# Optimization experiments

Measured on AMD Instinct MI355X. Metric: run time of the kernel, lower is better.

The kernel has to match this reference:

```python
import jax, jax.numpy as jnp
import numpy as np

B, T, I, H, L = 128, 512, 64, 512, 64  # batch, seq_len, input=latent size, hidden
DEC_STEPS = 100  # hardcoded in the original decoder loop


def _lstm_cell(x, h, c, Wih, Whh, bih, bhh):
    # PyTorch gate order: i, f, g, o
    gates = x @ Wih.T + h @ Whh.T + bih + bhh  # [B, 4H]
    i, f, g, o = jnp.split(gates, 4, axis=-1)
    c = jax.nn.sigmoid(f) * c + jax.nn.sigmoid(i) * jnp.tanh(g)
    h = jax.nn.sigmoid(o) * jnp.tanh(c)
    return h, c


def setup_inputs() -> dict:
    key = jax.random.key(0)
    ks = jax.random.split(key, 18)
    u = lambda k, shape, fan: jax.random.uniform(k, shape, jnp.float32, -1.0, 1.0) / np.sqrt(fan).astype(np.float32)
    return {
        "sequences": jax.random.normal(ks[0], (B, T, I), jnp.float32),
        "seq_lengths": jnp.full((B,), T, dtype=jnp.int32),
        "eps": jax.random.normal(ks[1], (B, L), jnp.float32),
        "W_ih_enc": u(ks[2], (4 * H, I), H), "W_hh_enc": u(ks[3], (4 * H, H), H),
        "b_ih_enc": u(ks[4], (4 * H,), H), "b_hh_enc": u(ks[5], (4 * H,), H),
        "W_mean": u(ks[6], (L, H), H), "b_mean": u(ks[7], (L,), H),
        "W_logvar": u(ks[8], (L, H), H), "b_logvar": u(ks[9], (L,), H),
        "W_init": u(ks[10], (H, L), L), "b_init": u(ks[11], (H,), L),
        "W_ih_dec": u(ks[12], (4 * H, I), H), "W_hh_dec": u(ks[13], (4 * H, H), H),
        "b_ih_dec": u(ks[14], (4 * H,), H), "b_hh_dec": u(ks[15], (4 * H,), H),
        "W_out": u(ks[16], (I, H), H), "b_out": u(ks[17], (I,), H),
    }


def _forward(sequences, eps,
             W_ih_enc, W_hh_enc, b_ih_enc, b_hh_enc,
             W_mean, b_mean, W_logvar, b_logvar,
             W_init, b_init,
             W_ih_dec, W_hh_dec, b_ih_dec, b_hh_dec,
             W_out, b_out):
    Bn = sequences.shape[0]
    h0 = jnp.zeros((Bn, H), sequences.dtype)

    # ---- encoder: full-sequence LSTM, keep only final hidden state ----
    def enc_step(carry, x_t):
        h, c = carry
        h, c = _lstm_cell(x_t, h, c, W_ih_enc, W_hh_enc, b_ih_enc, b_hh_enc)
        return (h, c), None

    (h_n, _), _ = jax.lax.scan(enc_step, (h0, h0), sequences.transpose(1, 0, 2))

    # ---- VAE reparameterization ----
    mean = h_n @ W_mean.T + b_mean
    log_var = h_n @ W_logvar.T + b_logvar
    z = mean + eps * jnp.exp(0.5 * log_var)

    h_dec = z @ W_init.T + b_init
    c_dec = jnp.zeros_like(h_dec)
    x0 = jnp.zeros((Bn, L), z.dtype)

    def dec_step(carry, _):
        h, c, x = carry
        h, c = _lstm_cell(x, h, c, W_ih_dec, W_hh_dec, b_ih_dec, b_hh_dec)
        x_hat = h @ W_out.T + b_out
        return (h, c, x_hat), x_hat

    _, xs = jax.lax.scan(dec_step, (h_dec, c_dec, x0), None, length=DEC_STEPS)
    x_hat = xs.transpose(1, 0, 2)  # [B, 100, I]
    return x_hat, mean, log_var


def reference(sequences, seq_lengths, eps,
              W_ih_enc, W_hh_enc, b_ih_enc, b_hh_enc,
              W_mean, b_mean, W_logvar, b_logvar,
              W_init, b_init,
              W_ih_dec, W_hh_dec, b_ih_dec, b_hh_dec,
              W_out, b_out):
    del seq_lengths  # accepted but unused by the original forward
    return _forward(sequences, eps,
                    W_ih_enc, W_hh_enc, b_ih_enc, b_hh_enc,
                    W_mean, b_mean, W_logvar, b_logvar,
                    W_init, b_init,
                    W_ih_dec, W_hh_dec, b_ih_dec, b_hh_dec,
                    W_out, b_out)
```

## Files before the change

kernel.cpp:

```cpp
#include <hip/hip_runtime.h>
#include <stdint.h>


typedef short short8 __attribute__((ext_vector_type(8)));
typedef float f32x4 __attribute__((ext_vector_type(4)));
typedef unsigned int u32x4 __attribute__((ext_vector_type(4)));

#define WS_FLAGS  0
#define WS_HBUF0  16384
#define WS_HBUF1  147456
#define WS_Z      278528
#define WS_BCOMB  311296
#define WS_WCOMB  319488
#define WS_SEQB   2416640
#define WS_END    10805248
#define WS_ZERO   WS_HBUF1
#define HB1_SIZE  131072

static __device__ __forceinline__ float b2f(unsigned short u) {
    return __builtin_bit_cast(float, (unsigned int)u << 16);
}
static __device__ __forceinline__ unsigned short f2b(float f) {
    unsigned int u = __builtin_bit_cast(unsigned int, f);
    unsigned int r = u + 0x7FFFu + ((u >> 16) & 1u);
    return (unsigned short)(r >> 16);
}
static __device__ __forceinline__ float sigm(float x)  { return 1.0f / (1.0f + __expf(-x)); }
static __device__ __forceinline__ float tanhx(float x) { return 1.0f - 2.0f / (__expf(2.0f * x) + 1.0f); }

static __device__ __forceinline__ short8 cvt8(const float* p) {
    const float4 a = ((const float4*)p)[0];
    const float4 b = ((const float4*)p)[1];
    short8 r;
    r[0] = (short)f2b(a.x); r[1] = (short)f2b(a.y);
    r[2] = (short)f2b(a.z); r[3] = (short)f2b(a.w);
    r[4] = (short)f2b(b.x); r[5] = (short)f2b(b.y);
    r[6] = (short)f2b(b.z); r[7] = (short)f2b(b.w);
    return r;
}

static __device__ __forceinline__ uint32_t phase_of(uint32_t R) {
    return (R <= 512u) ? ((R >> 1) & 1u)
                       : ((((R - 513u) >> 1) & 1u) ^ 1u);
}

static __device__ __forceinline__ int alperm(int u) { return u ^ ((u >> 3) & 7); }

static __device__ __forceinline__ void load2x16_cc(const void* p0, const void* p1,
                                                   u32x4& v0, u32x4& v1) {
    asm volatile("global_load_dwordx4 %0, %2, off sc0 sc1\n\t"
                 "global_load_dwordx4 %1, %3, off sc0 sc1\n\t"
                 "s_waitcnt vmcnt(0)"
                 : "=&v"(v0), "=&v"(v1) : "v"(p0), "v"(p1) : "memory");
}
static __device__ __forceinline__ void store16_cc(void* p, u32x4 v) {
    asm volatile("global_store_dwordx4 %0, %1, off sc0 sc1"
                 :: "v"(p), "v"(v) : "memory");
}
static __device__ __forceinline__ void drain_vm() {
    asm volatile("s_waitcnt vmcnt(0)" ::: "memory");
}

__global__ void __launch_bounds__(256)
seqcvt_kernel(const float* __restrict__ src, unsigned short* __restrict__ dst)
{
    int i = (blockIdx.x * 256 + threadIdx.x) * 4;
    float4 v = *(const float4*)(src + i);
    uint32_t lo = (uint32_t)f2b(v.x) | ((uint32_t)f2b(v.y) << 16);
    uint32_t hi = (uint32_t)f2b(v.z) | ((uint32_t)f2b(v.w) << 16);
    uint2 o; o.x = lo; o.y = hi;
    *(uint2*)(dst + i) = o;
}

__global__ void __launch_bounds__(256)
wcomb_kernel(const float* __restrict__ Wih_d,
             const float* __restrict__ Whh_d,
             const float* __restrict__ Wout,
             const float* __restrict__ bih_d,
             const float* __restrict__ bhh_d,
             const float* __restrict__ bout,
             unsigned char* __restrict__ ws)
{
    __shared__ float Ash[64][64];
    __shared__ float Bsh[64][65];
    const int bid = blockIdx.x, t = threadIdx.x;
    const int gt0 = (bid >> 3) * 64, ht0 = (bid & 7) * 64;
    for (int j = 0; j < 16; ++j) {
        int idx = t + j * 256;
        int r = idx >> 6, c = idx & 63;
        Ash[r][c] = Wih_d[(size_t)(gt0 + r) * 64 + c];
        Bsh[r][c] = Wout[(size_t)r * 512 + ht0 + c];
    }
    __syncthreads();
    const int gl = t >> 2, hl0 = (t & 3) * 16;
    for (int hh = 0; hh < 16; ++hh) {
        float acc = 0.f;
        #pragma unroll
        for (int i = 0; i < 64; ++i) acc += Ash[gl][i] * Bsh[i][hl0 + hh];
        int g = gt0 + gl, h = ht0 + hl0 + hh;
        float v = Whh_d[(size_t)g * 512 + h] + acc;
        ((unsigned short*)(ws + WS_WCOMB))[(size_t)g * 512 + h] = f2b(v);
    }
    if ((bid & 7) == 0 && t < 64) {
        int g = gt0 + t;
        float acc = bih_d[g] + bhh_d[g];
        #pragma unroll
        for (int i = 0; i < 64; ++i) acc += bout[i] * Ash[t][i];
        ((float*)(ws + WS_BCOMB))[g] = acc;
    }
}

__global__ void __launch_bounds__(512, 2)
vae_persistent(const float* __restrict__ seq,
               const unsigned short* __restrict__ seqb,
               const float* __restrict__ eps,
               const float* __restrict__ Wih_e,
               const float* __restrict__ Whh_e,
               const float* __restrict__ bih_e,
               const float* __restrict__ bhh_e,
               const float* __restrict__ Wmean,
               const float* __restrict__ bmean,
               const float* __restrict__ Wlv,
               const float* __restrict__ blv,
               const float* __restrict__ Winit,
               const float* __restrict__ binit,
               const float* __restrict__ Whh_d,
               const float* __restrict__ bih_d,
               const float* __restrict__ bhh_d,
               const float* __restrict__ Wout,
               const float* __restrict__ bout,
               unsigned char* __restrict__ ws,
               float* __restrict__ out)
{
    __shared__ __align__(16) short Al[16 * 520];
    __shared__ __align__(16) short Ho[16 * 36];
    __shared__ float fbuf[128];
    __shared__ float zl[16 * 64];

    const int tid  = threadIdx.x;
    const int g    = blockIdx.x & 7;
    const int s    = blockIdx.x >> 3;
    const int b0   = g * 16;
    const int lane = tid & 63;
    const int wv   = tid >> 6;
    const int col  = lane & 15;
    const int q    = lane >> 4;
    const int nloc = wv * 16 + col;
    const int gt   = nloc & 3;
    const int grow = gt * 512 + s * 32 + (nloc >> 2);

    uint32_t* flags = (uint32_t*)(ws + WS_FLAGS) + (size_t)g * 512;
    unsigned char* hbuf0 = ws + WS_HBUF0;
    unsigned char* hbuf1 = ws + WS_HBUF1;
    uint32_t* zbuf = (uint32_t*)(ws + WS_Z);

    float cst[4] = {0.f, 0.f, 0.f, 0.f};

    int aoff[16];
    #pragma unroll
    for (int kt = 0; kt < 16; ++kt)
        aoff[kt] = col * 520 + alperm(kt * 4 + q) * 8;
    const int stg_b  = tid >> 5;
    const int stg_c  = tid & 31;
    const int stg_u0 = alperm(stg_c * 2);

    auto wait_and_stage = [&](uint32_t R, bool guard) {
        if (guard) __syncthreads();
        const unsigned char* src = (R & 1) ? hbuf1 : hbuf0;
        const uint32_t pm = phase_of(R) ? 0x40004000u : 0u;
        const unsigned char* p0 = src + (size_t)(b0 + stg_b) * 1024 + stg_c * 32;
        u32x4 v0, v1;
        uint32_t tries = 0;
        for (;;) {
            load2x16_cc(p0, p0 + 16, v0, v1);
            uint32_t bad = 0;
            #pragma unroll
            for (int i = 0; i < 4; ++i) {
                bad |= (v0[i] & 0x40004000u) ^ pm;
                bad |= (v1[i] & 0x40004000u) ^ pm;
            }
            if (bad == 0) break;
            if (tries == 1)      __builtin_amdgcn_s_sleep(1);
            else if (tries == 2) __builtin_amdgcn_s_sleep(2);
            else if (tries == 3 || tries == 4) __builtin_amdgcn_s_sleep(4);
            else if (tries >= 5) __builtin_amdgcn_s_sleep(8);
            ++tries;
        }
        #pragma unroll
        for (int i = 0; i < 4; ++i) { v0[i] ^= pm; v1[i] ^= pm; }
        u32x4* dst = (u32x4*)Al;
        dst[stg_b * 65 + stg_u0]       = v0;
        dst[stg_b * 65 + (stg_u0 ^ 1)] = v1;
        __syncthreads();
    };

    auto publish_h = [&](uint32_t R) {
        if (wv == 0) {
            unsigned char* dst = (R & 1) ? hbuf1 : hbuf0;
            const uint32_t pm = phase_of(R) ? 0x40004000u : 0u;
            int row = lane >> 2, part = lane & 3;
            const short* hp = Ho + row * 36 + part * 8;
            uint2 lo = *(const uint2*)(hp);
            uint2 hi = *(const uint2*)(hp + 4);
            u32x4 v; v[0] = lo.x; v[1] = lo.y; v[2] = hi.x; v[3] = hi.y;
            #pragma unroll
            for (int i = 0; i < 4; ++i) v[i] ^= pm;
            store16_cc(dst + (size_t)(b0 + row) * 1024 + s * 64 + part * 16, v);
        }
    };

    short8 wfrag[16];
    auto load_wfrag_f32 = [&](const float* Wsrc) {
        #pragma unroll
        for (int kt = 0; kt < 16; ++kt)
            wfrag[kt] = cvt8(Wsrc + (size_t)grow * 512 + kt * 32 + q * 8);
    };
    auto load_wfrag_bf16 = [&](const unsigned short* Wsrc) {
        #pragma unroll
        for (int kt = 0; kt < 16; ++kt)
            wfrag[kt] = *(const short8*)((const short*)Wsrc +
                         (size_t)grow * 512 + kt * 32 + q * 8);
    };

    auto cell_update = [&](f32x4 acc) {
        float act[4];
        #pragma unroll
        for (int r = 0; r < 4; ++r)
            act[r] = (gt == 2) ? tanhx(acc[r]) : sigm(acc[r]);
        int base = lane & ~3;
        #pragma unroll
        for (int r = 0; r < 4; ++r) {
            float vi = __shfl(act[r], base + 0);
            float vf = __shfl(act[r], base + 1);
            float vg = __shfl(act[r], base + 2);
            float vo = __shfl(act[r], base + 3);
            cst[r] = vf * cst[r] + vi * vg;
            act[r] = vo * tanhx(cst[r]);
        }
        if (gt == 0) {
            int hd4 = wv * 4 + (col >> 2);
            #pragma unroll
            for (int r = 0; r < 4; ++r)
                Ho[(q * 4 + r) * 36 + hd4] = (short)f2b(act[r]);
        }
    };

    load_wfrag_f32(Whh_e);
    short8 xwf[2];
    #pragma unroll
    for (int kt = 0; kt < 2; ++kt)
        xwf[kt] = cvt8(Wih_e + (size_t)grow * 64 + kt * 32 + q * 8);
    const float bias_e = bih_e[grow] + bhh_e[grow];

    auto load_x = [&](int t, short8* xf) {
        if (seqb) {
            const short* xs = (const short*)seqb + ((size_t)(b0 + col) * 512 + t) * 64 + q * 8;
            xf[0] = *(const short8*)(xs);
            xf[1] = *(const short8*)(xs + 32);
        } else {
            const float* xs = seq + ((size_t)(b0 + col) * 512 + t) * 64 + q * 8;
            xf[0] = cvt8(xs);
            xf[1] = cvt8(xs + 32);
        }
    };

    short8 xf[2];
    load_x(0, xf);
    for (uint32_t t = 0; t < 512; ++t) {
        f32x4 acc = {bias_e, bias_e, bias_e, bias_e};
        acc = __builtin_amdgcn_mfma_f32_16x16x32_bf16(xf[0], xwf[0], acc, 0, 0, 0);
        acc = __builtin_amdgcn_mfma_f32_16x16x32_bf16(xf[1], xwf[1], acc, 0, 0, 0);
        if (t < 511) load_x(t + 1, xf);
        wait_and_stage(t, false);
        f32x4 acc1 = {0.f, 0.f, 0.f, 0.f};
        #pragma unroll
        for (int kt = 0; kt < 16; kt += 2) {
            short8 a0 = *(const short8*)(Al + aoff[kt]);
            short8 a1 = *(const short8*)(Al + aoff[kt + 1]);
            acc  = __builtin_amdgcn_mfma_f32_16x16x32_bf16(a0, wfrag[kt],     acc,  0, 0, 0);
            acc1 = __builtin_amdgcn_mfma_f32_16x16x32_bf16(a1, wfrag[kt + 1], acc1, 0, 0, 0);
        }
        #pragma unroll
        for (int r = 0; r < 4; ++r) acc[r] += acc1[r];
        cell_update(acc);
        __syncthreads();
        publish_h(t + 1);
    }

    wait_and_stage(512, false);
    if (tid < 128) {
        int which = tid >> 6, idx = tid & 63;
        int b = idx >> 2, ldl = idx & 3;
        int ld = s * 4 + ldl;
        const float* wrow = (which ? Wlv : Wmean) + (size_t)ld * 512;
        float a = (which ? blv[ld] : bmean[ld]);
        for (int u = 0; u < 64; ++u) {
            const short* ap = Al + b * 520 + alperm(u) * 8;
            const float* wp = wrow + u * 8;
            #pragma unroll
            for (int e = 0; e < 8; ++e)
                a += b2f((unsigned short)ap[e]) * wp[e];
        }
        out[819200 + which * 8192 + (size_t)(b0 + b) * 64 + ld] = a;
        fbuf[which * 64 + idx] = a;
    }
    __syncthreads();
    if (wv == 0) {
        int b = lane >> 2, ldl = lane & 3;
        int ld = s * 4 + ldl;
        float m = fbuf[lane], lv = fbuf[64 + lane];
        float e = eps[(size_t)(b0 + b) * 64 + ld];
        float z = m + e * __expf(0.5f * lv);
        __hip_atomic_store(zbuf + (size_t)(b0 + b) * 64 + ld,
                           __builtin_bit_cast(uint32_t, z),
                           __ATOMIC_RELAXED, __HIP_MEMORY_SCOPE_AGENT);
        drain_vm();
        if (lane == 0)
            __hip_atomic_store(&flags[s * 32], 513u,
                               __ATOMIC_RELAXED, __HIP_MEMORY_SCOPE_AGENT);
    }
    if (wv == 0 && lane < 16)
        while (__hip_atomic_load(&flags[lane * 32], __ATOMIC_RELAXED,
                                 __HIP_MEMORY_SCOPE_AGENT) < 513u) {}
    __syncthreads();

    #pragma unroll
    for (int j = 0; j < 2; ++j) {
        int idx = tid + j * 512;
        int b = idx >> 6, l = idx & 63;
        uint32_t v = __hip_atomic_load(zbuf + (size_t)(b0 + b) * 64 + l,
                                       __ATOMIC_RELAXED, __HIP_MEMORY_SCOPE_AGENT);
        zl[b * 64 + l] = __builtin_bit_cast(float, v);
    }
    __syncthreads();
    {
        int b = tid >> 5, c = tid & 31;
        #pragma unroll
        for (int j = 0; j < 16; ++j) {
            int hd = c * 16 + j;
            float a = binit[hd];
            const float* wr = Winit + (size_t)hd * 64;
            #pragma unroll
            for (int l = 0; l < 64; ++l) a += zl[b * 64 + l] * wr[l];
            Al[b * 520 + alperm(c * 2 + (j >> 3)) * 8 + (j & 7)] = (short)f2b(a);
        }
    }
    #pragma unroll
    for (int r = 0; r < 4; ++r) cst[r] = 0.f;
    __syncthreads();

    short8 wof[16];
    float xbias = 0.f;
    if (s < 4 && wv == 7) {
        xbias = bout[s * 16 + col];
        #pragma unroll
        for (int kt = 0; kt < 16; ++kt)
            wof[kt] = cvt8(Wout + (size_t)(s * 16 + col) * 512 + kt * 32 + q * 8);
    }
    auto xhat_emit = [&](int d) {
        f32x4 a2 = {xbias, xbias, xbias, xbias};
        #pragma unroll
        for (int kt = 0; kt < 16; ++kt) {
            short8 a = *(const short8*)(Al + aoff[kt]);
            a2 = __builtin_amdgcn_mfma_f32_16x16x32_bf16(a, wof[kt], a2, 0, 0, 0);
        }
        #pragma unroll
        for (int r = 0; r < 4; ++r) {
            int b = q * 4 + r;
            out[((size_t)(b0 + b) * 100 + d) * 64 + s * 16 + col] = a2[r];
        }
    };

    load_wfrag_f32(Whh_d);
    float bias = bih_d[grow] + bhh_d[grow];
    for (uint32_t d = 0; d < 100; ++d) {
        if (d > 0) wait_and_stage(513 + d, true);
        f32x4 acc = {bias, bias, bias, bias};
        f32x4 acc1 = {0.f, 0.f, 0.f, 0.f};
        #pragma unroll
        for (int kt = 0; kt < 16; kt += 2) {
            short8 a0 = *(const short8*)(Al + aoff[kt]);
            short8 a1 = *(const short8*)(Al + aoff[kt + 1]);
            acc  = __builtin_amdgcn_mfma_f32_16x16x32_bf16(a0, wfrag[kt],     acc,  0, 0, 0);
            acc1 = __builtin_amdgcn_mfma_f32_16x16x32_bf16(a1, wfrag[kt + 1], acc1, 0, 0, 0);
        }
        #pragma unroll
        for (int r = 0; r < 4; ++r) acc[r] += acc1[r];
        cell_update(acc);
        __syncthreads();
        publish_h(514 + d);
        if (d >= 1 && s < 4 && wv == 7) xhat_emit(d - 1);
        if (d == 0) {
            load_wfrag_bf16((const unsigned short*)(ws + WS_WCOMB));
            bias = ((const float*)(ws + WS_BCOMB))[grow];
        }
    }
    wait_and_stage(613, true);
    if (s < 4 && wv == 7) xhat_emit(99);
}

extern "C" void kernel_launch(void* const* d_in, const int* in_sizes, int n_in,
                              void* d_out, int out_size, void* d_ws, size_t ws_size,
                              hipStream_t stream) {
    (void)in_sizes; (void)n_in; (void)out_size;
    const float* seq   = (const float*)d_in[0];
    const float* eps   = (const float*)d_in[2];
    const float* Wih_e = (const float*)d_in[3];
    const float* Whh_e = (const float*)d_in[4];
    const float* bih_e = (const float*)d_in[5];
    const float* bhh_e = (const float*)d_in[6];
    const float* Wmean = (const float*)d_in[7];
    const float* bmean = (const float*)d_in[8];
    const float* Wlv   = (const float*)d_in[9];
    const float* blv   = (const float*)d_in[10];
    const float* Winit = (const float*)d_in[11];
    const float* binit = (const float*)d_in[12];
    const float* Wih_d = (const float*)d_in[13];
    const float* Whh_d = (const float*)d_in[14];
    const float* bih_d = (const float*)d_in[15];
    const float* bhh_d = (const float*)d_in[16];
    const float* Wout  = (const float*)d_in[17];
    const float* bout  = (const float*)d_in[18];
    unsigned char* ws = (unsigned char*)d_ws;
    float* out = (float*)d_out;

    const bool have_seqb = ws_size >= (size_t)WS_END;
    unsigned short* seqb = have_seqb ? (unsigned short*)(ws + WS_SEQB) : nullptr;

    hipMemsetAsync(ws, 0, WS_ZERO, stream);
    hipMemsetAsync(ws + WS_HBUF1, 0x40, HB1_SIZE, stream);
    if (have_seqb)
        seqcvt_kernel<<<4096, 256, 0, stream>>>(seq, seqb);
    wcomb_kernel<<<256, 256, 0, stream>>>(Wih_d, Whh_d, Wout, bih_d, bhh_d, bout, ws);
    vae_persistent<<<128, 512, 0, stream>>>(
        seq, seqb, eps, Wih_e, Whh_e, bih_e, bhh_e,
        Wmean, bmean, Wlv, blv, Winit, binit,
        Whh_d, bih_d, bhh_d, Wout, bout, ws, out);
}
```

Baseline: 1.731 ms.

## Double-buffer staged hidden state and publish h directly from registers via shuffles

Splits the LDS staging buffer into two halves alternated by step parity, so the leading __syncthreads before staging can be dropped. The cell update now gathers h values with wave shuffles and stores them straight to the global exchange buffer, removing the Ho LDS round trip and the __syncthreads before publishing. The spin backoff is also capped at a shorter sleep. This cuts per-step barriers on the latency-bound recurrent critical path, in exchange for more, smaller global stores from every wave and a reliance on parity double-buffering to stay race-free.

```diff
diff --git a/kernel.cpp b/kernel.cpp
--- a/kernel.cpp
+++ b/kernel.cpp
@@ -5,6 +5,7 @@
 typedef short short8 __attribute__((ext_vector_type(8)));
 typedef float f32x4 __attribute__((ext_vector_type(4)));
 typedef unsigned int u32x4 __attribute__((ext_vector_type(4)));
+typedef unsigned int u32x2 __attribute__((ext_vector_type(2)));
 
 #define WS_FLAGS  0
 #define WS_HBUF0  16384
@@ -17,6 +18,8 @@
 #define WS_ZERO   WS_HBUF1
 #define HB1_SIZE  131072
 
+#define AL_HALF   8320
+
 static __device__ __forceinline__ float b2f(unsigned short u) {
     return __builtin_bit_cast(float, (unsigned int)u << 16);
 }
@@ -52,10 +55,6 @@
                  "global_load_dwordx4 %1, %3, off sc0 sc1\n\t"
                  "s_waitcnt vmcnt(0)"
                  : "=&v"(v0), "=&v"(v1) : "v"(p0), "v"(p1) : "memory");
-}
-static __device__ __forceinline__ void store16_cc(void* p, u32x4 v) {
-    asm volatile("global_store_dwordx4 %0, %1, off sc0 sc1"
-                 :: "v"(p), "v"(v) : "memory");
 }
 static __device__ __forceinline__ void drain_vm() {
     asm volatile("s_waitcnt vmcnt(0)" ::: "memory");
@@ -132,8 +131,7 @@
                unsigned char* __restrict__ ws,
                float* __restrict__ out)
 {
-    __shared__ __align__(16) short Al[16 * 520];
-    __shared__ __align__(16) short Ho[16 * 36];
+    __shared__ __align__(16) short Al[2 * AL_HALF];
     __shared__ float fbuf[128];
     __shared__ float zl[16 * 64];
 
@@ -164,8 +162,7 @@
     const int stg_c  = tid & 31;
     const int stg_u0 = alperm(stg_c * 2);
 
-    auto wait_and_stage = [&](uint32_t R, bool guard) {
-        if (guard) __syncthreads();
+    auto wait_and_stage = [&](uint32_t R) {
         const unsigned char* src = (R & 1) ? hbuf1 : hbuf0;
         const uint32_t pm = phase_of(R) ? 0x40004000u : 0u;
         const unsigned char* p0 = src + (size_t)(b0 + stg_b) * 1024 + stg_c * 32;
@@ -182,47 +179,18 @@
             if (bad == 0) break;
             if (tries == 1)      __builtin_amdgcn_s_sleep(1);
             else if (tries == 2) __builtin_amdgcn_s_sleep(2);
-            else if (tries == 3 || tries == 4) __builtin_amdgcn_s_sleep(4);
-            else if (tries >= 5) __builtin_amdgcn_s_sleep(8);
+            else if (tries >= 3) __builtin_amdgcn_s_sleep(4);
             ++tries;
         }
         #pragma unroll
         for (int i = 0; i < 4; ++i) { v0[i] ^= pm; v1[i] ^= pm; }
-        u32x4* dst = (u32x4*)Al;
+        u32x4* dst = (u32x4*)(Al + (R & 1) * AL_HALF);
         dst[stg_b * 65 + stg_u0]       = v0;
         dst[stg_b * 65 + (stg_u0 ^ 1)] = v1;
         __syncthreads();
     };
 
-    auto publish_h = [&](uint32_t R) {
-        if (wv == 0) {
-            unsigned char* dst = (R & 1) ? hbuf1 : hbuf0;
-            const uint32_t pm = phase_of(R) ? 0x40004000u : 0u;
-            int row = lane >> 2, part = lane & 3;
-            const short* hp = Ho + row * 36 + part * 8;
-            uint2 lo = *(const uint2*)(hp);
-            uint2 hi = *(const uint2*)(hp + 4);
-            u32x4 v; v[0] = lo.x; v[1] = lo.y; v[2] = hi.x; v[3] = hi.y;
-            #pragma unroll
-            for (int i = 0; i < 4; ++i) v[i] ^= pm;
-            store16_cc(dst + (size_t)(b0 + row) * 1024 + s * 64 + part * 16, v);
-        }
-    };
-
-    short8 wfrag[16];
-    auto load_wfrag_f32 = [&](const float* Wsrc) {
-        #pragma unroll
-        for (int kt = 0; kt < 16; ++kt)
-            wfrag[kt] = cvt8(Wsrc + (size_t)grow * 512 + kt * 32 + q * 8);
-    };
-    auto load_wfrag_bf16 = [&](const unsigned short* Wsrc) {
-        #pragma unroll
-        for (int kt = 0; kt < 16; ++kt)
-            wfrag[kt] = *(const short8*)((const short*)Wsrc +
-                         (size_t)grow * 512 + kt * 32 + q * 8);
-    };
-
-    auto cell_update = [&](f32x4 acc) {
+    auto cell_publish = [&](f32x4 acc, uint32_t R) {
         float act[4];
         #pragma unroll
         for (int r = 0; r < 4; ++r)
@@ -237,12 +205,38 @@
             cst[r] = vf * cst[r] + vi * vg;
             act[r] = vo * tanhx(cst[r]);
         }
-        if (gt == 0) {
-            int hd4 = wv * 4 + (col >> 2);
-            #pragma unroll
-            for (int r = 0; r < 4; ++r)
-                Ho[(q * 4 + r) * 36 + hd4] = (short)f2b(act[r]);
-        }
+        unsigned char* dst = (R & 1) ? hbuf1 : hbuf0;
+        const uint32_t pm = phase_of(R) ? 0x40004000u : 0u;
+        const int qb = lane & 48;
+        #pragma unroll
+        for (int r = 0; r < 4; ++r) {
+            uint32_t u = (uint32_t)f2b(act[r]);
+            uint32_t g0 = (uint32_t)__shfl((int)u, qb + 0);
+            uint32_t g1 = (uint32_t)__shfl((int)u, qb + 4);
+            uint32_t g2 = (uint32_t)__shfl((int)u, qb + 8);
+            uint32_t g3 = (uint32_t)__shfl((int)u, qb + 12);
+            if (col == r) {
+                u32x2 pk;
+                pk[0] = (g0 | (g1 << 16)) ^ pm;
+                pk[1] = (g2 | (g3 << 16)) ^ pm;
+                void* p = dst + (size_t)(b0 + q * 4 + r) * 1024 + s * 64 + wv * 8;
+                asm volatile("global_store_dwordx2 %0, %1, off sc0 sc1"
+                             :: "v"(p), "v"(pk) : "memory");
+            }
+        }
+    };
+
+    short8 wfrag[16];
+    auto load_wfrag_f32 = [&](const float* Wsrc) {
+        #pragma unroll
+        for (int kt = 0; kt < 16; ++kt)
+            wfrag[kt] = cvt8(Wsrc + (size_t)grow * 512 + kt * 32 + q * 8);
+    };
+    auto load_wfrag_bf16 = [&](const unsigned short* Wsrc) {
+        #pragma unroll
+        for (int kt = 0; kt < 16; ++kt)
+            wfrag[kt] = *(const short8*)((const short*)Wsrc +
+                         (size_t)grow * 512 + kt * 32 + q * 8);
     };
 
     load_wfrag_f32(Whh_e);
@@ -271,23 +265,22 @@
         acc = __builtin_amdgcn_mfma_f32_16x16x32_bf16(xf[0], xwf[0], acc, 0, 0, 0);
         acc = __builtin_amdgcn_mfma_f32_16x16x32_bf16(xf[1], xwf[1], acc, 0, 0, 0);
         if (t < 511) load_x(t + 1, xf);
-        wait_and_stage(t, false);
+        wait_and_stage(t);
+        const short* ab = Al + (t & 1) * AL_HALF;
         f32x4 acc1 = {0.f, 0.f, 0.f, 0.f};
         #pragma unroll
         for (int kt = 0; kt < 16; kt += 2) {
-            short8 a0 = *(const short8*)(Al + aoff[kt]);
-            short8 a1 = *(const short8*)(Al + aoff[kt + 1]);
+            short8 a0 = *(const short8*)(ab + aoff[kt]);
+            short8 a1 = *(const short8*)(ab + aoff[kt + 1]);
             acc  = __builtin_amdgcn_mfma_f32_16x16x32_bf16(a0, wfrag[kt],     acc,  0, 0, 0);
             acc1 = __builtin_amdgcn_mfma_f32_16x16x32_bf16(a1, wfrag[kt + 1], acc1, 0, 0, 0);
         }
         #pragma unroll
         for (int r = 0; r < 4; ++r) acc[r] += acc1[r];
-        cell_update(acc);
-        __syncthreads();
-        publish_h(t + 1);
-    }
-
-    wait_and_stage(512, false);
+        cell_publish(acc, t + 1);
+    }
+
+    wait_and_stage(512);
     if (tid < 128) {
         int which = tid >> 6, idx = tid & 63;
         int b = idx >> 2, ldl = idx & 3;
@@ -342,7 +335,7 @@
             const float* wr = Winit + (size_t)hd * 64;
             #pragma unroll
             for (int l = 0; l < 64; ++l) a += zl[b * 64 + l] * wr[l];
-            Al[b * 520 + alperm(c * 2 + (j >> 3)) * 8 + (j & 7)] = (short)f2b(a);
+            Al[AL_HALF + b * 520 + alperm(c * 2 + (j >> 3)) * 8 + (j & 7)] = (short)f2b(a);
         }
     }
     #pragma unroll
@@ -357,11 +350,11 @@
         for (int kt = 0; kt < 16; ++kt)
             wof[kt] = cvt8(Wout + (size_t)(s * 16 + col) * 512 + kt * 32 + q * 8);
     }
-    auto xhat_emit = [&](int d) {
+    auto xhat_emit = [&](int d, const short* ab) {
         f32x4 a2 = {xbias, xbias, xbias, xbias};
         #pragma unroll
         for (int kt = 0; kt < 16; ++kt) {
-            short8 a = *(const short8*)(Al + aoff[kt]);
+            short8 a = *(const short8*)(ab + aoff[kt]);
             a2 = __builtin_amdgcn_mfma_f32_16x16x32_bf16(a, wof[kt], a2, 0, 0, 0);
         }
         #pragma unroll
@@ -374,29 +367,29 @@
     load_wfrag_f32(Whh_d);
     float bias = bih_d[grow] + bhh_d[grow];
     for (uint32_t d = 0; d < 100; ++d) {
-        if (d > 0) wait_and_stage(513 + d, true);
+        const uint32_t Rin = 513 + d;
+        if (d > 0) wait_and_stage(Rin);
+        const short* ab = Al + (Rin & 1) * AL_HALF;
         f32x4 acc = {bias, bias, bias, bias};
         f32x4 acc1 = {0.f, 0.f, 0.f, 0.f};
         #pragma unroll
         for (int kt = 0; kt < 16; kt += 2) {
-            short8 a0 = *(const short8*)(Al + aoff[kt]);
-            short8 a1 = *(const short8*)(Al + aoff[kt + 1]);
+            short8 a0 = *(const short8*)(ab + aoff[kt]);
+            short8 a1 = *(const short8*)(ab + aoff[kt + 1]);
             acc  = __builtin_amdgcn_mfma_f32_16x16x32_bf16(a0, wfrag[kt],     acc,  0, 0, 0);
             acc1 = __builtin_amdgcn_mfma_f32_16x16x32_bf16(a1, wfrag[kt + 1], acc1, 0, 0, 0);
         }
         #pragma unroll
         for (int r = 0; r < 4; ++r) acc[r] += acc1[r];
-        cell_update(acc);
-        __syncthreads();
-        publish_h(514 + d);
-        if (d >= 1 && s < 4 && wv == 7) xhat_emit(d - 1);
+        cell_publish(acc, 514 + d);
+        if (d >= 1 && s < 4 && wv == 7) xhat_emit(d - 1, ab);
         if (d == 0) {
             load_wfrag_bf16((const unsigned short*)(ws + WS_WCOMB));
             bias = ((const float*)(ws + WS_BCOMB))[grow];
         }
     }
-    wait_and_stage(613, true);
-    if (s < 4 && wv == 7) xhat_emit(99);
+    wait_and_stage(613);
+    if (s < 4 && wv == 7) xhat_emit(99, Al + AL_HALF);
 }
 
 extern "C" void kernel_launch(void* const* d_in, const int* in_sizes, int n_in,
```

Result: slower. 3.307 ms (+91.0%).
